# Kernel optimization log

Hardware: AMD Instinct MI355X
Metric: run time of the kernel (lower is better)

The kernel has to match this reference:

```python
import jax, jax.numpy as jnp
import numpy as np

N_FEAT = 350; D = 512; L = 4; DS = 64; NREG = 6; REG_E = 32
B = 32; S = 2048
CLAMP = 20.0


def _ln(x, g, b, eps=1e-5):
    mu = jnp.mean(x, axis=-1, keepdims=True)
    var = jnp.mean(jnp.square(x - mu), axis=-1, keepdims=True)
    return (x - mu) * jax.lax.rsqrt(var + eps) * g + b


def _slstm(x, ln_g, ln_b, Wi, bi, Wf, bf, Wz, bz, Wo, bo, Wp, bp):
    # x: [B,S,D] -> out: [B,S,D]
    xn = _ln(x, ln_g, ln_b)
    log_i = jnp.clip(jnp.einsum('bsd,de->bse', xn, Wi) + bi, -CLAMP, CLAMP)
    log_f = jnp.clip(jnp.einsum('bsd,de->bse', xn, Wf) + bf, -CLAMP, CLAMP)
    z = jnp.tanh(jnp.einsum('bsd,de->bse', xn, Wz) + bz)
    o = jax.nn.sigmoid(jnp.einsum('bsd,de->bse', xn, Wo) + bo)

    def step(carry, inp):
        m, c = carry
        li, lf, zt, ot = inp
        m_new = jnp.maximum(m + lf, li)
        i_s = jnp.exp(li - m_new)
        f_s = jnp.exp(m + lf - m_new)
        c_new = f_s * c + i_s * zt
        h = ot * jnp.tanh(c_new)
        return (m_new, c_new), h

    bsz = x.shape[0]
    init = (jnp.zeros((bsz, DS), x.dtype), jnp.zeros((bsz, DS), x.dtype))
    seq = (jnp.swapaxes(log_i, 0, 1), jnp.swapaxes(log_f, 0, 1),
           jnp.swapaxes(z, 0, 1), jnp.swapaxes(o, 0, 1))
    _, hs = jax.lax.scan(step, init, seq)  # hs: [S,B,DS]
    hs = jnp.swapaxes(hs, 0, 1)  # [B,S,DS]
    return jnp.einsum('bse,ed->bsd', hs, Wp) + bp


def setup_inputs() -> dict:
    key = jax.random.key(0)
    ks = iter(jax.random.split(key, 64))
    def p(*shape):
        return jax.random.normal(next(ks), shape, dtype=jnp.float32) * 0.02
    return {
        'x': jax.random.normal(next(ks), (B, S, N_FEAT), dtype=jnp.float32),
        'regime_ids': jax.random.randint(next(ks), (B, S), 0, NREG),
        'emb_regime': p(NREG, REG_E),
        'grn_w1': p(N_FEAT + REG_E, D), 'grn_b1': jnp.zeros((D,), jnp.float32),
        'grn_w2': p(D, N_FEAT), 'grn_b2': jnp.zeros((N_FEAT,), jnp.float32),
        'in_w': p(N_FEAT, D), 'in_b': jnp.zeros((D,), jnp.float32),
        'ln_in_g': jnp.ones((L, D), jnp.float32), 'ln_in_b': jnp.zeros((L, D), jnp.float32),
        'wi': p(L, D, DS), 'bi': jnp.zeros((L, DS), jnp.float32),
        'wf': p(L, D, DS), 'bf': jnp.zeros((L, DS), jnp.float32),
        'wz': p(L, D, DS), 'bz': jnp.zeros((L, DS), jnp.float32),
        'wo': p(L, D, DS), 'bo': jnp.zeros((L, DS), jnp.float32),
        'wp': p(L, DS, D), 'bp': jnp.zeros((L, D), jnp.float32),
        'nm_g': jnp.ones((L, D), jnp.float32), 'nm_b': jnp.zeros((L, D), jnp.float32),
        'hd15_w': p(D, 1), 'hd15_b': jnp.zeros((1,), jnp.float32),
        'hd30_w': p(D, 1), 'hd30_b': jnp.zeros((1,), jnp.float32),
        'hv_w': p(D, 3), 'hv_b': jnp.zeros((3,), jnp.float32),
        'hreg_w': p(D, NREG), 'hreg_b': jnp.zeros((NREG,), jnp.float32),
        'hrng_w': p(D, 3), 'hrng_b': jnp.zeros((3,), jnp.float32),
    }


def reference(x, regime_ids, emb_regime, grn_w1, grn_b1, grn_w2, grn_b2,
              in_w, in_b, ln_in_g, ln_in_b, wi, bi, wf, bf, wz, bz, wo, bo,
              wp, bp, nm_g, nm_b, hd15_w, hd15_b, hd30_w, hd30_b,
              hv_w, hv_b, hreg_w, hreg_b, hrng_w, hrng_b):
    # Variable selection network (regime-conditioned feature weights)
    remb = emb_regime[regime_ids]                      # [B,S,32]
    comb = jnp.concatenate([x, remb], axis=-1)         # [B,S,382]
    hidden = jax.nn.elu(jnp.einsum('bsf,fd->bsd', comb, grn_w1) + grn_b1)
    weights = jax.nn.softmax(jnp.einsum('bsd,df->bsf', hidden, grn_w2) + grn_b2, axis=-1)
    xw = x * weights
    h = jnp.einsum('bsf,fd->bsd', xw, in_w) + in_b     # [B,S,D]
    for l in range(L):
        res = _slstm(h, ln_in_g[l], ln_in_b[l], wi[l], bi[l], wf[l], bf[l],
                     wz[l], bz[l], wo[l], bo[l], wp[l], bp[l])
        h = _ln(h + res, nm_g[l], nm_b[l])
    h_last = h[:, -1, :]
    return (jnp.squeeze(h_last @ hd15_w + hd15_b, -1),
            jnp.squeeze(h_last @ hd30_w + hd30_b, -1),
            h_last @ hv_w + hv_b,
            h_last @ hreg_w + hreg_b,
            h_last @ hrng_w + hrng_b,
            h_last,
            weights[:, -1, :])
```

## Files before the change

kernel.cpp:

```cpp
#include <hip/hip_runtime.h>
#include <cmath>

#define NFEAT 350
#define DMODEL 512
#define NLAYER 4
#define DSZ 64
#define REG_E 32
#define BATCH 32
#define SEQ 2048
#define MTOK (BATCH * SEQ)
#define CLAMP_V 20.0f

#define CHUNK 64
#define NCHUNK (SEQ / CHUNK)

typedef short bf16x8 __attribute__((ext_vector_type(8)));
typedef float f32x4 __attribute__((ext_vector_type(4)));

__device__ __forceinline__ unsigned short f2b(float v) {
    union { float f; unsigned int u; } x; x.f = v;
    unsigned int r = x.u + 0x7fffu + ((x.u >> 16) & 1u);
    return (unsigned short)(r >> 16);
}
__device__ __forceinline__ float b2f(unsigned short u) {
    union { unsigned int i; float f; } x; x.i = ((unsigned int)u) << 16;
    return x.f;
}
__device__ __forceinline__ unsigned int pack2(float a, float b) {
    return ((unsigned int)f2b(b) << 16) | f2b(a);
}

__global__ __launch_bounds__(256) void tconv_k(const float* __restrict__ src,
                                               unsigned short* __restrict__ dst,
                                               int K, int N, int Kpad) {
    int k = blockIdx.x * 256 + threadIdx.x;
    int n = blockIdx.y;
    if (k >= Kpad) return;
    float v = (k < K && n < N) ? src[(size_t)k * N + n] : 0.f;
    dst[(size_t)n * Kpad + k] = f2b(v);
}

__global__ __launch_bounds__(256) void tconv_g_k(const float* __restrict__ wi,
                                                 const float* __restrict__ wf,
                                                 const float* __restrict__ wz,
                                                 const float* __restrict__ wo,
                                                 unsigned short* __restrict__ dst) {
    int k = blockIdx.x * 256 + threadIdx.x;
    int n = blockIdx.y;
    int z = blockIdx.z;
    int l = z >> 2, g = z & 3;
    const float* src = (g == 0 ? wi : g == 1 ? wf : g == 2 ? wz : wo) + (size_t)l * DMODEL * DSZ;
    dst[(size_t)z * 32768 + (size_t)n * 512 + k] = f2b(src[(size_t)k * DSZ + n]);
}

__global__ __launch_bounds__(1024) void gbias_k(const float* bi, const float* bf_,
                                                const float* bz, const float* bo,
                                                float* __restrict__ gbias) {
    int t = threadIdx.x;
    int l = t >> 8, r = t & 255, g = r >> 6, e = r & 63;
    const float* s = (g == 0 ? bi : g == 1 ? bf_ : g == 2 ? bz : bo);
    gbias[t] = s[l * 64 + e];
}

__global__ __launch_bounds__(256) void build_xc_k(const float* __restrict__ x,
                                                  const int* __restrict__ rid,
                                                  const float* __restrict__ emb,
                                                  unsigned short* __restrict__ xc) {
    int i = blockIdx.x * 256 + threadIdx.x;
    int m = i / 192, p = i - m * 192;
    int k = p * 2;
    float a = 0.f, b = 0.f;
    if (k < 350) {
        const float2 v = *(const float2*)(x + (size_t)m * NFEAT + k);
        a = v.x; b = v.y;
    } else if (k < 382) {
        int r = rid[m];
        const float2 v = *(const float2*)(emb + r * REG_E + (k - 350));
        a = v.x; b = v.y;
    }
    ((unsigned int*)xc)[(size_t)m * 192 + p] = pack2(a, b);
}

template <int ALD, int EPI>
__global__ __launch_bounds__(256) void mgemm_k(const unsigned short* __restrict__ Ab,
                                               const float* __restrict__ Af,
                                               const unsigned short* __restrict__ Bt,
                                               const float* __restrict__ bias,
                                               float* __restrict__ Cf,
                                               unsigned short* __restrict__ Cb,
                                               const float* __restrict__ muA,
                                               const float* __restrict__ rstdA,
                                               const float* __restrict__ lng,
                                               const float* __restrict__ lnb,
                                               int lda, int ldb, int K, int N, int ldc) {
    __shared__ unsigned short As[128][40];
    __shared__ unsigned short Bs[128][40];
    const int tid = threadIdx.x;
    const int lane = tid & 63;
    const int wave = tid >> 6;
    const int l15 = lane & 15;
    const int quad = lane >> 4;
    const int wm = (wave >> 1) * 64;
    const int wn = (wave & 1) * 64;
    const size_t m0 = (size_t)blockIdx.y * 128;
    const int n0 = blockIdx.x * 128;

    const int sr = tid >> 2;
    const int ku = tid & 3;

    const unsigned short* Br0 = Bt + ((size_t)(n0 + sr)) * ldb + ku * 8;
    const unsigned short* Br1 = Br0 + (size_t)64 * ldb;

    const unsigned short* Ar0 = nullptr;
    const unsigned short* Ar1 = nullptr;
    const float* Fr0 = nullptr;
    const float* Fr1 = nullptr;
    float mu0 = 0.f, rs0 = 0.f, mu1 = 0.f, rs1 = 0.f;
    if (ALD == 0) {
        Ar0 = Ab + (m0 + sr) * (size_t)lda + ku * 8;
        Ar1 = Ar0 + (size_t)64 * lda;
    } else {
        Fr0 = Af + (m0 + sr) * (size_t)lda + ku * 8;
        Fr1 = Fr0 + (size_t)64 * lda;
        mu0 = muA[m0 + sr];   rs0 = rstdA[m0 + sr];
        mu1 = muA[m0 + sr + 64]; rs1 = rstdA[m0 + sr + 64];
    }

    f32x4 acc[4][4] = {};

    for (int k0 = 0; k0 < K; k0 += 32) {
        if (ALD == 0) {
            *(uint4*)&As[sr][ku * 8]      = *(const uint4*)(Ar0 + k0);
            *(uint4*)&As[sr + 64][ku * 8] = *(const uint4*)(Ar1 + k0);
        } else {
            float4 g0 = *(const float4*)(lng + k0 + ku * 8);
            float4 g1 = *(const float4*)(lng + k0 + ku * 8 + 4);
            float4 c0 = *(const float4*)(lnb + k0 + ku * 8);
            float4 c1 = *(const float4*)(lnb + k0 + ku * 8 + 4);
            {
                float4 v0 = *(const float4*)(Fr0 + k0);
                float4 v1 = *(const float4*)(Fr0 + k0 + 4);
                uint4 w;
                w.x = pack2((v0.x - mu0) * rs0 * g0.x + c0.x, (v0.y - mu0) * rs0 * g0.y + c0.y);
                w.y = pack2((v0.z - mu0) * rs0 * g0.z + c0.z, (v0.w - mu0) * rs0 * g0.w + c0.w);
                w.z = pack2((v1.x - mu0) * rs0 * g1.x + c1.x, (v1.y - mu0) * rs0 * g1.y + c1.y);
                w.w = pack2((v1.z - mu0) * rs0 * g1.z + c1.z, (v1.w - mu0) * rs0 * g1.w + c1.w);
                *(uint4*)&As[sr][ku * 8] = w;
            }
            {
                float4 v0 = *(const float4*)(Fr1 + k0);
                float4 v1 = *(const float4*)(Fr1 + k0 + 4);
                uint4 w;
                w.x = pack2((v0.x - mu1) * rs1 * g0.x + c0.x, (v0.y - mu1) * rs1 * g0.y + c0.y);
                w.y = pack2((v0.z - mu1) * rs1 * g0.z + c0.z, (v0.w - mu1) * rs1 * g0.w + c0.w);
                w.z = pack2((v1.x - mu1) * rs1 * g1.x + c1.x, (v1.y - mu1) * rs1 * g1.y + c1.y);
                w.w = pack2((v1.z - mu1) * rs1 * g1.z + c1.z, (v1.w - mu1) * rs1 * g1.w + c1.w);
                *(uint4*)&As[sr + 64][ku * 8] = w;
            }
        }
        *(uint4*)&Bs[sr][ku * 8]      = *(const uint4*)(Br0 + k0);
        *(uint4*)&Bs[sr + 64][ku * 8] = *(const uint4*)(Br1 + k0);
        __syncthreads();
        bf16x8 af[4], bf[4];
#pragma unroll
        for (int mt = 0; mt < 4; mt++)
            af[mt] = *(const bf16x8*)&As[wm + mt * 16 + l15][quad * 8];
#pragma unroll
        for (int nt = 0; nt < 4; nt++)
            bf[nt] = *(const bf16x8*)&Bs[wn + nt * 16 + l15][quad * 8];
#pragma unroll
        for (int mt = 0; mt < 4; mt++)
#pragma unroll
            for (int nt = 0; nt < 4; nt++)
                acc[mt][nt] = __builtin_amdgcn_mfma_f32_16x16x32_bf16(af[mt], bf[nt], acc[mt][nt], 0, 0, 0);
        __syncthreads();
    }

#pragma unroll
    for (int mt = 0; mt < 4; mt++) {
        int gmb = wm + mt * 16 + quad * 4;
#pragma unroll
        for (int nt = 0; nt < 4; nt++) {
            int gn = n0 + wn + nt * 16 + l15;
            if (gn < N) {
                float bv = bias[gn];
#pragma unroll
                for (int r = 0; r < 4; r++) {
                    size_t gm = m0 + gmb + r;
                    float v = acc[mt][nt][r] + bv;
                    if (EPI == 0) {
                        v = v > 0.f ? v : expm1f(v);
                        Cb[gm * (size_t)ldc + gn] = f2b(v);
                    } else if (EPI == 1) {
                        Cb[gm * (size_t)ldc + gn] = f2b(v);
                    } else if (EPI == 2) {
                        int g = gn >> 6;
                        if (g < 2) v = fminf(fmaxf(v, -CLAMP_V), CLAMP_V);
                        else if (g == 2) v = tanhf(v);
                        else v = 1.f / (1.f + expf(-v));
                        Cf[gm * (size_t)ldc + gn] = v;
                    } else {
                        Cf[gm * (size_t)ldc + gn] = v;
                    }
                }
            }
        }
    }
}

__global__ __launch_bounds__(256) void softmax_xw_k(const unsigned short* __restrict__ logits,
                                                    unsigned short* __restrict__ xc,
                                                    float* __restrict__ out_wlast) {
    int tok = blockIdx.x * 4 + (threadIdx.x >> 6);
    int lane = threadIdx.x & 63;
    const unsigned short* lr = logits + (size_t)tok * NFEAT;
    unsigned short* xr = xc + (size_t)tok * 384;
    float v[6];
    float mx = -1e30f;
#pragma unroll
    for (int i = 0; i < 6; i++) {
        int idx = lane + 64 * i;
        v[i] = (idx < NFEAT) ? b2f(lr[idx]) : -1e30f;
        mx = fmaxf(mx, v[i]);
    }
#pragma unroll
    for (int o = 32; o > 0; o >>= 1) mx = fmaxf(mx, __shfl_xor(mx, o, 64));
    float s = 0.f;
#pragma unroll
    for (int i = 0; i < 6; i++) { v[i] = expf(v[i] - mx); s += v[i]; }
#pragma unroll
    for (int o = 32; o > 0; o >>= 1) s += __shfl_xor(s, o, 64);
    float inv = 1.f / s;
    bool last = ((tok & (SEQ - 1)) == SEQ - 1);
    int b = tok >> 11;
#pragma unroll
    for (int i = 0; i < 6; i++) {
        int idx = lane + 64 * i;
        if (idx < NFEAT) {
            float w = v[i] * inv;
            xr[idx] = f2b(w * b2f(xr[idx]));
            if (last) out_wlast[b * NFEAT + idx] = w;
        } else if (idx < 352) {
            xr[idx] = 0;
        }
    }
}

__global__ __launch_bounds__(256) void ln_stats_k(const float* __restrict__ h,
                                                  float* __restrict__ mu,
                                                  float* __restrict__ rstd) {
    int tok = blockIdx.x * 4 + (threadIdx.x >> 6);
    int lane = threadIdx.x & 63;
    const float* row = h + (size_t)tok * DMODEL;
    float s = 0.f, sq = 0.f;
#pragma unroll
    for (int i = 0; i < 8; i++) {
        float v = row[lane + 64 * i];
        s += v;
        sq += v * v;
    }
#pragma unroll
    for (int o = 32; o > 0; o >>= 1) {
        s += __shfl_xor(s, o, 64);
        sq += __shfl_xor(sq, o, 64);
    }
    if (lane == 0) {
        float m = s * (1.f / DMODEL);
        float var = sq * (1.f / DMODEL) - m * m;
        mu[tok] = m;
        rstd[tok] = rsqrtf(var + 1e-5f);
    }
}

__global__ __launch_bounds__(256) void seg_agg_k(const float* __restrict__ gates,
                                                 float* __restrict__ aggF,
                                                 float* __restrict__ aggL,
                                                 float* __restrict__ aggS) {
    int b = blockIdx.x >> 3;
    int cg = blockIdx.x & 7;
    int chunk = cg * 4 + (threadIdx.x >> 6);
    int e = threadIdx.x & 63;
    const float* gp = gates + ((size_t)b * SEQ + (size_t)chunk * CHUNK) * 256;
    float F = 0.f, L = -1e30f, s = 0.f;
#pragma unroll 4
    for (int t = 0; t < CHUNK; t++) {
        const float* q = gp + (size_t)t * 256;
        float li = q[e], lf = q[64 + e], z = q[128 + e];
        float Ln = fmaxf(L + lf, li);
        s = expf(L + lf - Ln) * s + expf(li - Ln) * z;
        L = Ln;
        F += lf;
    }
    int idx = (b * NCHUNK + chunk) * 64 + e;
    aggF[idx] = F; aggL[idx] = L; aggS[idx] = s;
}

__global__ __launch_bounds__(64) void chunk_scan_k(const float* __restrict__ aggF,
                                                   const float* __restrict__ aggL,
                                                   const float* __restrict__ aggS,
                                                   float* __restrict__ stM,
                                                   float* __restrict__ stC) {
    int b = blockIdx.x;
    int e = threadIdx.x;
    float m = 0.f, c = 0.f;
    for (int k = 0; k < NCHUNK; k++) {
        int idx = (b * NCHUNK + k) * 64 + e;
        stM[idx] = m; stC[idx] = c;
        float F = aggF[idx], L = aggL[idx], s = aggS[idx];
        float mn = fmaxf(m + F, L);
        c = expf(m + F - mn) * c + expf(L - mn) * s;
        m = mn;
    }
}

__global__ __launch_bounds__(256) void replay_k(const float* __restrict__ gates,
                                                const float* __restrict__ stM,
                                                const float* __restrict__ stC,
                                                float* __restrict__ hs) {
    int b = blockIdx.x >> 3;
    int cg = blockIdx.x & 7;
    int chunk = cg * 4 + (threadIdx.x >> 6);
    int e = threadIdx.x & 63;
    int s0 = chunk * CHUNK;
    const float* gp = gates + ((size_t)b * SEQ + s0) * 256;
    float* hp = hs + ((size_t)b * SEQ + s0) * DSZ;
    int idx = (b * NCHUNK + chunk) * 64 + e;
    float m = stM[idx], c = stC[idx];
#pragma unroll 4
    for (int t = 0; t < CHUNK; t++) {
        const float* q = gp + (size_t)t * 256;
        float li = q[e], lf = q[64 + e], z = q[128 + e], o = q[192 + e];
        float mlf = m + lf;
        float mn = fmaxf(mlf, li);
        c = expf(mlf - mn) * c + expf(li - mn) * z;
        m = mn;
        hp[(size_t)t * DSZ + e] = o * tanhf(c);
    }
}

__global__ __launch_bounds__(256) void outproj_k(const float* __restrict__ hs,
                                                 const float* __restrict__ wp,
                                                 const float* __restrict__ bp,
                                                 const float* __restrict__ nmg,
                                                 const float* __restrict__ nmb,
                                                 float* __restrict__ h,
                                                 float* __restrict__ mu,
                                                 float* __restrict__ rstd) {
    __shared__ float shs[16][DSZ];
    __shared__ float swp[16][DMODEL];
    int wv = threadIdx.x >> 6;
    int lane = threadIdx.x & 63;
    int tok0 = blockIdx.x * 16;

    {
        const float4* src = (const float4*)(hs + (size_t)tok0 * DSZ);
        ((float4*)&shs[0][0])[threadIdx.x] = src[threadIdx.x];
    }
    __syncthreads();

    float acc[4][8] = {};
    for (int k0 = 0; k0 < DSZ; k0 += 16) {
        const float4* src = (const float4*)(wp + (size_t)k0 * DMODEL);
#pragma unroll
        for (int i = 0; i < 8; i++)
            ((float4*)&swp[0][0])[threadIdx.x + i * 256] = src[threadIdx.x + i * 256];
        __syncthreads();
#pragma unroll
        for (int k = 0; k < 16; k++) {
            float bv[8];
#pragma unroll
            for (int j = 0; j < 8; j++) bv[j] = swp[k][lane + 64 * j];
#pragma unroll
            for (int t = 0; t < 4; t++) {
                float av = shs[wv * 4 + t][k0 + k];
#pragma unroll
                for (int j = 0; j < 8; j++) acc[t][j] += av * bv[j];
            }
        }
        __syncthreads();
    }

#pragma unroll
    for (int t = 0; t < 4; t++) {
        int tok = tok0 + wv * 4 + t;
        float u[8];
        float s = 0.f, sq = 0.f;
#pragma unroll
        for (int j = 0; j < 8; j++) {
            int col = lane + 64 * j;
            float v = h[(size_t)tok * DMODEL + col] + acc[t][j] + bp[col];
            u[j] = v;
            s += v; sq += v * v;
        }
#pragma unroll
        for (int o = 32; o > 0; o >>= 1) { s += __shfl_xor(s, o, 64); sq += __shfl_xor(sq, o, 64); }
        float mean = s * (1.f / DMODEL);
        float var = sq * (1.f / DMODEL) - mean * mean;
        float rs = rsqrtf(var + 1e-5f);
        float s2 = 0.f, sq2 = 0.f;
#pragma unroll
        for (int j = 0; j < 8; j++) {
            int col = lane + 64 * j;
            float v = (u[j] - mean) * rs * nmg[col] + nmb[col];
            h[(size_t)tok * DMODEL + col] = v;
            s2 += v; sq2 += v * v;
        }
#pragma unroll
        for (int o = 32; o > 0; o >>= 1) { s2 += __shfl_xor(s2, o, 64); sq2 += __shfl_xor(sq2, o, 64); }
        if (lane == 0) {
            float m2 = s2 * (1.f / DMODEL);
            float v2 = sq2 * (1.f / DMODEL) - m2 * m2;
            mu[tok] = m2;
            rstd[tok] = rsqrtf(v2 + 1e-5f);
        }
    }
}

__global__ __launch_bounds__(64) void heads_k(const float* __restrict__ h,
                                              const float* hd15_w, const float* hd15_b,
                                              const float* hd30_w, const float* hd30_b,
                                              const float* hv_w, const float* hv_b,
                                              const float* hreg_w, const float* hreg_b,
                                              const float* hrng_w, const float* hrng_b,
                                              float* __restrict__ out) {
    int b = blockIdx.x;
    int lane = threadIdx.x;
    __shared__ float row[DMODEL];
    const float* hp = h + (size_t)(b * SEQ + SEQ - 1) * DMODEL;
#pragma unroll
    for (int i = 0; i < 8; i++) row[lane + 64 * i] = hp[lane + 64 * i];
    __syncthreads();
#pragma unroll
    for (int i = 0; i < 8; i++) out[448 + b * DMODEL + lane + 64 * i] = row[lane + 64 * i];
    if (lane < 14) {
        const float* w; const float* bb;
        int ncol, j, off;
        if (lane == 0)      { w = hd15_w; bb = hd15_b; ncol = 1; j = 0;         off = 0 + b; }
        else if (lane == 1) { w = hd30_w; bb = hd30_b; ncol = 1; j = 0;         off = 32 + b; }
        else if (lane < 5)  { j = lane - 2;  w = hv_w;   bb = hv_b;   ncol = 3; off = 64 + b * 3 + j; }
        else if (lane < 11) { j = lane - 5;  w = hreg_w; bb = hreg_b; ncol = 6; off = 160 + b * 6 + j; }
        else                { j = lane - 11; w = hrng_w; bb = hrng_b; ncol = 3; off = 352 + b * 3 + j; }
        float s = bb[j];
        for (int k = 0; k < DMODEL; k++) s += row[k] * w[k * ncol + j];
        out[off] = s;
    }
}

extern "C" void kernel_launch(void* const* d_in, const int* in_sizes, int n_in,
                              void* d_out, int out_size, void* d_ws, size_t ws_size,
                              hipStream_t stream) {
    (void)in_sizes; (void)n_in; (void)out_size; (void)ws_size;
    const float* x      = (const float*)d_in[0];
    const int*   rid    = (const int*)d_in[1];
    const float* emb    = (const float*)d_in[2];
    const float* grn_w1 = (const float*)d_in[3];
    const float* grn_b1 = (const float*)d_in[4];
    const float* grn_w2 = (const float*)d_in[5];
    const float* grn_b2 = (const float*)d_in[6];
    const float* in_w   = (const float*)d_in[7];
    const float* in_b   = (const float*)d_in[8];
    const float* ln_g   = (const float*)d_in[9];
    const float* ln_b   = (const float*)d_in[10];
    const float* wi     = (const float*)d_in[11];
    const float* bi     = (const float*)d_in[12];
    const float* wf     = (const float*)d_in[13];
    const float* bf_    = (const float*)d_in[14];
    const float* wz     = (const float*)d_in[15];
    const float* bz     = (const float*)d_in[16];
    const float* wo     = (const float*)d_in[17];
    const float* bo     = (const float*)d_in[18];
    const float* wp     = (const float*)d_in[19];
    const float* bp     = (const float*)d_in[20];
    const float* nm_g   = (const float*)d_in[21];
    const float* nm_b   = (const float*)d_in[22];

    float* out = (float*)d_out;
    char* W = (char*)d_ws;

    float* h               = (float*)W;
    unsigned short* hidden = (unsigned short*)W;
    unsigned short* logits = (unsigned short*)(W + 67108864);
    char* RB = W + 134217728;
    unsigned short* xc = (unsigned short*)RB;
    float* gates  = (float*)RB;
    float* hsbuf  = (float*)(RB + 67108864);
    char* RM = W + 218103808;
    float* aggF  = (float*)(RM);
    float* aggL  = (float*)(RM + 262144);
    float* aggS  = (float*)(RM + 524288);
    float* stM   = (float*)(RM + 786432);
    float* stC   = (float*)(RM + 1048576);
    float* mu    = (float*)(RM + 1310720);
    float* rstd  = (float*)(RM + 1572864);
    unsigned short* w1t  = (unsigned short*)(RM + 1835008);
    unsigned short* w2t  = (unsigned short*)(RM + 2228224);
    unsigned short* inwt = (unsigned short*)(RM + 2621440);
    unsigned short* gwt  = (unsigned short*)(RM + 2981888);
    float* gbias         = (float*)(RM + 4030464);

    build_xc_k<<<MTOK * 192 / 256, 256, 0, stream>>>(x, rid, emb, xc);
    tconv_k<<<dim3(2, 512), 256, 0, stream>>>(grn_w1, w1t, 382, 512, 384);
    tconv_k<<<dim3(2, 384), 256, 0, stream>>>(grn_w2, w2t, 512, 350, 512);
    tconv_k<<<dim3(2, 512), 256, 0, stream>>>(in_w, inwt, 350, 512, 352);
    tconv_g_k<<<dim3(2, 64, 16), 256, 0, stream>>>(wi, wf, wz, wo, gwt);
    gbias_k<<<1, 1024, 0, stream>>>(bi, bf_, bz, bo, gbias);

    mgemm_k<0, 0><<<dim3(4, 512), 256, 0, stream>>>(xc, nullptr, w1t, grn_b1, nullptr, hidden,
                                                    nullptr, nullptr, nullptr, nullptr,
                                                    384, 384, 384, 512, 512);
    mgemm_k<0, 1><<<dim3(3, 512), 256, 0, stream>>>(hidden, nullptr, w2t, grn_b2, nullptr, logits,
                                                    nullptr, nullptr, nullptr, nullptr,
                                                    512, 512, 512, 350, 350);
    softmax_xw_k<<<MTOK / 4, 256, 0, stream>>>(logits, xc, out + 16832);
    mgemm_k<0, 3><<<dim3(4, 512), 256, 0, stream>>>(xc, nullptr, inwt, in_b, h, nullptr,
                                                    nullptr, nullptr, nullptr, nullptr,
                                                    384, 352, 352, 512, 512);
    ln_stats_k<<<MTOK / 4, 256, 0, stream>>>(h, mu, rstd);

    for (int l = 0; l < NLAYER; l++) {
        mgemm_k<1, 2><<<dim3(2, 512), 256, 0, stream>>>(nullptr, h, gwt + (size_t)l * 131072,
                                                        gbias + l * 256, gates, nullptr,
                                                        mu, rstd,
                                                        ln_g + l * DMODEL, ln_b + l * DMODEL,
                                                        512, 512, 512, 256, 256);
        seg_agg_k<<<BATCH * 8, 256, 0, stream>>>(gates, aggF, aggL, aggS);
        chunk_scan_k<<<BATCH, 64, 0, stream>>>(aggF, aggL, aggS, stM, stC);
        replay_k<<<BATCH * 8, 256, 0, stream>>>(gates, stM, stC, hsbuf);

        outproj_k<<<MTOK / 16, 256, 0, stream>>>(hsbuf,
                                                 wp + (size_t)l * DSZ * DMODEL,
                                                 bp + l * DMODEL,
                                                 nm_g + l * DMODEL,
                                                 nm_b + l * DMODEL,
                                                 h, mu, rstd);
    }

    heads_k<<<BATCH, 64, 0, stream>>>(h,
                                      (const float*)d_in[23], (const float*)d_in[24],
                                      (const float*)d_in[25], (const float*)d_in[26],
                                      (const float*)d_in[27], (const float*)d_in[28],
                                      (const float*)d_in[29], (const float*)d_in[30],
                                      (const float*)d_in[31], (const float*)d_in[32],
                                      out);
}
```

Before: 1.347 ms.

## Use split-bf16 MFMA for sLSTM output projection with fused residual layernorm

Replaces the FP32 FMA outer-product output projection with a bf16 MFMA kernel. Both the hidden states and Wp are split into hi/lo bf16 pairs and three MFMA terms are summed to keep near-FP32 accuracy. The replay kernel now writes the hi/lo bf16 hidden states, and a new pre-pass transposes Wp into the split layout. The residual layernorm and stats are reduced across waves through shared memory. The extra MFMA terms and the doubled hs storage cost some work, in exchange for moving the matmul onto matrix cores.

```diff
diff --git a/kernel.cpp b/kernel.cpp
--- a/kernel.cpp
+++ b/kernel.cpp
@@ -38,6 +38,21 @@
     if (k >= Kpad) return;
     float v = (k < K && n < N) ? src[(size_t)k * N + n] : 0.f;
     dst[(size_t)n * Kpad + k] = f2b(v);
+}
+
+__global__ __launch_bounds__(256) void tconv_wp_k(const float* __restrict__ wp,
+                                                  unsigned short* __restrict__ dst) {
+    int idx = blockIdx.x * 256 + threadIdx.x;
+    int l = idx >> 15;
+    int rem = idx & 32767;
+    int n = rem >> 6;
+    int k = rem & 63;
+    float v = wp[((size_t)l * 64 + k) * 512 + n];
+    unsigned short hi = f2b(v);
+    unsigned short lo = f2b(v - b2f(hi));
+    unsigned short* d = dst + ((size_t)l * 512 + n) * 128;
+    d[k] = hi;
+    d[64 + k] = lo;
 }
 
 __global__ __launch_bounds__(256) void tconv_g_k(const float* __restrict__ wi,
@@ -316,14 +331,14 @@
 __global__ __launch_bounds__(256) void replay_k(const float* __restrict__ gates,
                                                 const float* __restrict__ stM,
                                                 const float* __restrict__ stC,
-                                                float* __restrict__ hs) {
+                                                unsigned short* __restrict__ hs) {
     int b = blockIdx.x >> 3;
     int cg = blockIdx.x & 7;
     int chunk = cg * 4 + (threadIdx.x >> 6);
     int e = threadIdx.x & 63;
     int s0 = chunk * CHUNK;
     const float* gp = gates + ((size_t)b * SEQ + s0) * 256;
-    float* hp = hs + ((size_t)b * SEQ + s0) * DSZ;
+    unsigned short* hp = hs + ((size_t)b * SEQ + s0) * 128;
     int idx = (b * NCHUNK + chunk) * 64 + e;
     float m = stM[idx], c = stC[idx];
 #pragma unroll 4
@@ -334,85 +349,108 @@
         float mn = fmaxf(mlf, li);
         c = expf(mlf - mn) * c + expf(li - mn) * z;
         m = mn;
-        hp[(size_t)t * DSZ + e] = o * tanhf(c);
-    }
-}
-
-__global__ __launch_bounds__(256) void outproj_k(const float* __restrict__ hs,
-                                                 const float* __restrict__ wp,
-                                                 const float* __restrict__ bp,
-                                                 const float* __restrict__ nmg,
-                                                 const float* __restrict__ nmb,
-                                                 float* __restrict__ h,
-                                                 float* __restrict__ mu,
-                                                 float* __restrict__ rstd) {
-    __shared__ float shs[16][DSZ];
-    __shared__ float swp[16][DMODEL];
-    int wv = threadIdx.x >> 6;
-    int lane = threadIdx.x & 63;
-    int tok0 = blockIdx.x * 16;
+        float v = o * tanhf(c);
+        unsigned short hi = f2b(v);
+        hp[(size_t)t * 128 + e] = hi;
+        hp[(size_t)t * 128 + 64 + e] = f2b(v - b2f(hi));
+    }
+}
+
+__global__ __launch_bounds__(512) void outproj_mfma_k(const unsigned short* __restrict__ hs,
+                                                      const unsigned short* __restrict__ wpt,
+                                                      const float* __restrict__ bp,
+                                                      const float* __restrict__ nmg,
+                                                      const float* __restrict__ nmb,
+                                                      float* __restrict__ h,
+                                                      float* __restrict__ mu,
+                                                      float* __restrict__ rstd) {
+    __shared__ unsigned short As[32][136];
+    __shared__ float sS[32][4], sQ[32][4];
+    __shared__ float sS2[32][4], sQ2[32][4];
+    const int tid = threadIdx.x;
+    const int lane = tid & 63;
+    const int wave = tid >> 6;
+    const int l15 = lane & 15;
+    const int quad = lane >> 4;
+    const int wm = (wave >> 2) * 16;
+    const int wn = (wave & 3) * 128;
+    const int cg = wave & 3;
+    const size_t tok0 = (size_t)blockIdx.x * 32;
 
     {
-        const float4* src = (const float4*)(hs + (size_t)tok0 * DSZ);
-        ((float4*)&shs[0][0])[threadIdx.x] = src[threadIdx.x];
+        int row = tid >> 4, ku = tid & 15;
+        *(uint4*)&As[row][ku * 8] = *(const uint4*)(hs + (tok0 + row) * 128 + ku * 8);
     }
     __syncthreads();
 
-    float acc[4][8] = {};
-    for (int k0 = 0; k0 < DSZ; k0 += 16) {
-        const float4* src = (const float4*)(wp + (size_t)k0 * DMODEL);
-#pragma unroll
-        for (int i = 0; i < 8; i++)
-            ((float4*)&swp[0][0])[threadIdx.x + i * 256] = src[threadIdx.x + i * 256];
-        __syncthreads();
-#pragma unroll
-        for (int k = 0; k < 16; k++) {
-            float bv[8];
-#pragma unroll
-            for (int j = 0; j < 8; j++) bv[j] = swp[k][lane + 64 * j];
-#pragma unroll
-            for (int t = 0; t < 4; t++) {
-                float av = shs[wv * 4 + t][k0 + k];
-#pragma unroll
-                for (int j = 0; j < 8; j++) acc[t][j] += av * bv[j];
+    f32x4 acc[8] = {};
+#pragma unroll 1
+    for (int term = 0; term < 3; term++) {
+        const int aoff = (term == 2) ? 64 : 0;
+        const int boff = (term == 1) ? 64 : 0;
+#pragma unroll
+        for (int ks = 0; ks < 2; ks++) {
+            bf16x8 af = *(const bf16x8*)&As[wm + l15][aoff + ks * 32 + quad * 8];
+#pragma unroll
+            for (int nt = 0; nt < 8; nt++) {
+                bf16x8 bv = *(const bf16x8*)(wpt + (size_t)(wn + nt * 16 + l15) * 128 + boff + ks * 32 + quad * 8);
+                acc[nt] = __builtin_amdgcn_mfma_f32_16x16x32_bf16(af, bv, acc[nt], 0, 0, 0);
             }
         }
-        __syncthreads();
-    }
-
-#pragma unroll
-    for (int t = 0; t < 4; t++) {
-        int tok = tok0 + wv * 4 + t;
-        float u[8];
+    }
+
+    float bpv[8], gv[8], bv_[8];
+#pragma unroll
+    for (int nt = 0; nt < 8; nt++) {
+        int col = wn + nt * 16 + l15;
+        bpv[nt] = bp[col]; gv[nt] = nmg[col]; bv_[nt] = nmb[col];
+    }
+
+#pragma unroll
+    for (int r = 0; r < 4; r++) {
+        int trow = wm + quad * 4 + r;
+        const float* hrow = h + (tok0 + trow) * (size_t)DMODEL;
         float s = 0.f, sq = 0.f;
 #pragma unroll
-        for (int j = 0; j < 8; j++) {
-            int col = lane + 64 * j;
-            float v = h[(size_t)tok * DMODEL + col] + acc[t][j] + bp[col];
-            u[j] = v;
-            s += v; sq += v * v;
+        for (int nt = 0; nt < 8; nt++) {
+            float u = acc[nt][r] + bpv[nt] + hrow[wn + nt * 16 + l15];
+            acc[nt][r] = u;
+            s += u; sq += u * u;
         }
 #pragma unroll
-        for (int o = 32; o > 0; o >>= 1) { s += __shfl_xor(s, o, 64); sq += __shfl_xor(sq, o, 64); }
+        for (int o = 8; o > 0; o >>= 1) { s += __shfl_xor(s, o, 64); sq += __shfl_xor(sq, o, 64); }
+        if (l15 == 0) { sS[trow][cg] = s; sQ[trow][cg] = sq; }
+    }
+    __syncthreads();
+
+#pragma unroll
+    for (int r = 0; r < 4; r++) {
+        int trow = wm + quad * 4 + r;
+        float s = sS[trow][0] + sS[trow][1] + sS[trow][2] + sS[trow][3];
+        float sq = sQ[trow][0] + sQ[trow][1] + sQ[trow][2] + sQ[trow][3];
         float mean = s * (1.f / DMODEL);
         float var = sq * (1.f / DMODEL) - mean * mean;
         float rs = rsqrtf(var + 1e-5f);
+        float* hrow = h + (tok0 + trow) * (size_t)DMODEL;
         float s2 = 0.f, sq2 = 0.f;
 #pragma unroll
-        for (int j = 0; j < 8; j++) {
-            int col = lane + 64 * j;
-            float v = (u[j] - mean) * rs * nmg[col] + nmb[col];
-            h[(size_t)tok * DMODEL + col] = v;
+        for (int nt = 0; nt < 8; nt++) {
+            float v = (acc[nt][r] - mean) * rs * gv[nt] + bv_[nt];
+            hrow[wn + nt * 16 + l15] = v;
             s2 += v; sq2 += v * v;
         }
 #pragma unroll
-        for (int o = 32; o > 0; o >>= 1) { s2 += __shfl_xor(s2, o, 64); sq2 += __shfl_xor(sq2, o, 64); }
-        if (lane == 0) {
-            float m2 = s2 * (1.f / DMODEL);
-            float v2 = sq2 * (1.f / DMODEL) - m2 * m2;
-            mu[tok] = m2;
-            rstd[tok] = rsqrtf(v2 + 1e-5f);
-        }
+        for (int o = 8; o > 0; o >>= 1) { s2 += __shfl_xor(s2, o, 64); sq2 += __shfl_xor(sq2, o, 64); }
+        if (l15 == 0) { sS2[trow][cg] = s2; sQ2[trow][cg] = sq2; }
+    }
+    __syncthreads();
+    if (tid < 32) {
+        float s2 = sS2[tid][0] + sS2[tid][1] + sS2[tid][2] + sS2[tid][3];
+        float sq2 = sQ2[tid][0] + sQ2[tid][1] + sQ2[tid][2] + sQ2[tid][3];
+        float m2 = s2 * (1.f / DMODEL);
+        float v2 = sq2 * (1.f / DMODEL) - m2 * m2;
+        mu[tok0 + tid] = m2;
+        rstd[tok0 + tid] = rsqrtf(v2 + 1e-5f);
     }
 }
 
@@ -483,7 +521,7 @@
     char* RB = W + 134217728;
     unsigned short* xc = (unsigned short*)RB;
     float* gates  = (float*)RB;
-    float* hsbuf  = (float*)(RB + 67108864);
+    unsigned short* hsbuf = (unsigned short*)(RB + 67108864);
     char* RM = W + 218103808;
     float* aggF  = (float*)(RM);
     float* aggL  = (float*)(RM + 262144);
@@ -497,6 +535,7 @@
     unsigned short* inwt = (unsigned short*)(RM + 2621440);
     unsigned short* gwt  = (unsigned short*)(RM + 2981888);
     float* gbias         = (float*)(RM + 4030464);
+    unsigned short* wpt  = (unsigned short*)(RM + 4034560);
 
     build_xc_k<<<MTOK * 192 / 256, 256, 0, stream>>>(x, rid, emb, xc);
     tconv_k<<<dim3(2, 512), 256, 0, stream>>>(grn_w1, w1t, 382, 512, 384);
@@ -504,6 +543,7 @@
     tconv_k<<<dim3(2, 512), 256, 0, stream>>>(in_w, inwt, 350, 512, 352);
     tconv_g_k<<<dim3(2, 64, 16), 256, 0, stream>>>(wi, wf, wz, wo, gwt);
     gbias_k<<<1, 1024, 0, stream>>>(bi, bf_, bz, bo, gbias);
+    tconv_wp_k<<<512, 256, 0, stream>>>(wp, wpt);
 
     mgemm_k<0, 0><<<dim3(4, 512), 256, 0, stream>>>(xc, nullptr, w1t, grn_b1, nullptr, hidden,
                                                     nullptr, nullptr, nullptr, nullptr,
@@ -527,12 +567,12 @@
         chunk_scan_k<<<BATCH, 64, 0, stream>>>(aggF, aggL, aggS, stM, stC);
         replay_k<<<BATCH * 8, 256, 0, stream>>>(gates, stM, stC, hsbuf);
 
-        outproj_k<<<MTOK / 16, 256, 0, stream>>>(hsbuf,
-                                                 wp + (size_t)l * DSZ * DMODEL,
-                                                 bp + l * DMODEL,
-                                                 nm_g + l * DMODEL,
-                                                 nm_b + l * DMODEL,
-                                                 h, mu, rstd);
+        outproj_mfma_k<<<MTOK / 32, 512, 0, stream>>>(hsbuf,
+                                                      wpt + (size_t)l * 65536,
+                                                      bp + l * DMODEL,
+                                                      nm_g + l * DMODEL,
+                                                      nm_b + l * DMODEL,
+                                                      h, mu, rstd);
     }
 
     heads_k<<<BATCH, 64, 0, stream>>>(h,
```

Result: slower. 1.510 ms (+12.1%).
